# Kernel tuning notes

Measured on AMD Instinct MI355X. Metric: run time of the kernel, lower is better.

The kernel has to match this reference:

```python
import jax, jax.numpy as jnp
import numpy as np

B, L, HC, D = 4, 4096, 4, 1024
K, DIL = 4, 2
EPS = 1e-5
C = HC * D
PAD = (K - 1) * DIL


def setup_inputs() -> dict:
    key = jax.random.key(0)
    k1, k2, k3 = jax.random.split(key, 3)
    x = jax.random.normal(k1, (B, L, HC, D), dtype=jnp.float32)
    # RMSNorm affine weights, one per chunk (torch init: ones; randomize slightly for a
    # non-trivial baseline)
    norm_weight = 1.0 + 0.02 * jax.random.normal(k2, (HC, D), dtype=jnp.float32)
    # depthwise conv weight [C, 1, K] (torch init is zeros; use small random values so
    # the kernel-correctness baseline is non-degenerate)
    conv_weight = 0.1 * jax.random.normal(k3, (C, 1, K), dtype=jnp.float32)
    return {"x": x, "norm_weight": norm_weight, "conv_weight": conv_weight}


def reference(x, norm_weight, conv_weight):
    # per-chunk RMSNorm over last dim: [B, L, HC, D]
    ms = jnp.mean(jnp.square(x), axis=-1, keepdims=True)
    xn = x * jax.lax.rsqrt(ms + EPS) * norm_weight[None, None, :, :]
    # concat chunks along feature dim -> [B, L, C], then to [B, C, L]
    xc = xn.reshape(B, L, C).transpose(0, 2, 1)
    # depthwise dilated causal conv1d: left-pad (K-1)*DIL, output length L
    y = jax.lax.conv_general_dilated(
        xc, conv_weight,
        window_strides=(1,),
        padding=((PAD, 0),),
        rhs_dilation=(DIL,),
        feature_group_count=C,
        dimension_numbers=("NCH", "OIH", "NCH"),
    )
    y = jax.nn.silu(y)
    # back to [B, L, HC, D]
    return y.transpose(0, 2, 1).reshape(B, L, HC, D)
```

## Files before the change

### kernel.cpp

```cpp
#include <hip/hip_runtime.h>

namespace {

constexpr int B = 4, L = 4096, HC = 4, D = 1024, K = 4, DIL = 2;
constexpr int PAD = (K - 1) * DIL;
constexpr float EPS = 1e-5f;
constexpr int CL = 64;
constexpr int ST = 8;
constexpr int NSTEP = CL / ST;
constexpr int NT = L / CL;
constexpr int BDIM = 256;

__global__ __launch_bounds__(BDIM, 4) void engram_shortconv_stream(
    const float* __restrict__ x,
    const float* __restrict__ nw,
    const float* __restrict__ cw,
    float* __restrict__ out)
{
    __shared__ float s_part[ST][BDIM];
    __shared__ float s_inv[CL + PAD];

    const int blk = blockIdx.x;
    const int t   = blk % NT;
    const int hc  = (blk / NT) % HC;
    const int b   = blk / (NT * HC);
    const int l0  = t * CL;

    const int tid  = threadIdx.x;
    const int wave = tid >> 6;
    const int lane = tid & 63;

    const size_t rs = (size_t)HC * D;
    const float* xcol = x   + ((size_t)b * L * HC + (size_t)hc) * D + tid * 4;
    float*       ocol = out + ((size_t)b * L * HC + (size_t)hc) * D + tid * 4;

    const float4 nw4 = *(const float4*)(nw + (size_t)hc * D + tid * 4);
    const float nwv[4] = { nw4.x, nw4.y, nw4.z, nw4.w };
    float wk[4][4];
    #pragma unroll
    for (int j = 0; j < 4; ++j) {
        const float4 w = *(const float4*)(cw + ((size_t)hc * D + tid * 4 + j) * K);
        wk[j][0] = w.x * nwv[j]; wk[j][1] = w.y * nwv[j];
        wk[j][2] = w.z * nwv[j]; wk[j][3] = w.w * nwv[j];
    }

    float win[PAD][4];
    float pf[ST][4];

    #pragma unroll
    for (int r = 0; r < PAD; ++r) {
        const int l = l0 - PAD + r;
        float4 v = make_float4(0.f, 0.f, 0.f, 0.f);
        if (l >= 0) v = *(const float4*)(xcol + (size_t)l * rs);
        win[r][0] = v.x; win[r][1] = v.y; win[r][2] = v.z; win[r][3] = v.w;
    }
    #pragma unroll
    for (int r = 0; r < PAD; ++r)
        s_part[r][tid] = win[r][0]*win[r][0] + win[r][1]*win[r][1]
                       + win[r][2]*win[r][2] + win[r][3]*win[r][3];
    #pragma unroll
    for (int r = 0; r < ST; ++r) {
        const float4 v = *(const float4*)(xcol + (size_t)(l0 + r) * rs);
        pf[r][0] = v.x; pf[r][1] = v.y; pf[r][2] = v.z; pf[r][3] = v.w;
    }
    __syncthreads();
    for (int rr = wave; rr < PAD; rr += 4) {
        float s = s_part[rr][lane]       + s_part[rr][lane + 64]
                + s_part[rr][lane + 128] + s_part[rr][lane + 192];
        #pragma unroll
        for (int off = 32; off >= 1; off >>= 1) s += __shfl_xor(s, off);
        if (lane == 0) s_inv[rr] = rsqrtf(s * (1.0f / D) + EPS);
    }
    __syncthreads();
    #pragma unroll
    for (int r = 0; r < PAD; ++r) {
        const float iv = s_inv[r];
        win[r][0] *= iv; win[r][1] *= iv; win[r][2] *= iv; win[r][3] *= iv;
    }

    for (int s = 0; s < NSTEP; ++s) {
        const int base = l0 + s * ST;
        const int ib   = s * ST + PAD;

        #pragma unroll
        for (int r = 0; r < ST; ++r)
            s_part[r][tid] = pf[r][0]*pf[r][0] + pf[r][1]*pf[r][1]
                           + pf[r][2]*pf[r][2] + pf[r][3]*pf[r][3];
        __syncthreads();
        for (int rr = wave; rr < ST; rr += 4) {
            float sm = s_part[rr][lane]       + s_part[rr][lane + 64]
                     + s_part[rr][lane + 128] + s_part[rr][lane + 192];
            #pragma unroll
            for (int off = 32; off >= 1; off >>= 1) sm += __shfl_xor(sm, off);
            if (lane == 0) s_inv[ib + rr] = rsqrtf(sm * (1.0f / D) + EPS);
        }
        __syncthreads();

        #pragma unroll
        for (int r = 0; r < ST; ++r) {
            const float iv = s_inv[ib + r];
            pf[r][0] *= iv; pf[r][1] *= iv; pf[r][2] *= iv; pf[r][3] *= iv;
        }

        #pragma unroll
        for (int i = 0; i < ST; ++i) {
            float4 o; float* op = &o.x;
            #pragma unroll
            for (int j = 0; j < 4; ++j) {
                float a = 0.f;
                #pragma unroll
                for (int k = 0; k < 4; ++k) {
                    const int rel = i - 6 + 2 * k;
                    const float xv = (rel < 0) ? win[6 + rel][j] : pf[rel][j];
                    a = fmaf(wk[j][k], xv, a);
                }
                op[j] = a / (1.0f + __expf(-a));
            }
            *(float4*)(ocol + (size_t)(base + i) * rs) = o;
        }

        #pragma unroll
        for (int r = 0; r < PAD; ++r) {
            win[r][0] = pf[r + 2][0]; win[r][1] = pf[r + 2][1];
            win[r][2] = pf[r + 2][2]; win[r][3] = pf[r + 2][3];
        }

        if (s < NSTEP - 1) {
            #pragma unroll
            for (int r = 0; r < ST; ++r) {
                const float4 v = *(const float4*)(xcol + (size_t)(base + ST + r) * rs);
                pf[r][0] = v.x; pf[r][1] = v.y; pf[r][2] = v.z; pf[r][3] = v.w;
            }
        }
    }
}

}

extern "C" void kernel_launch(void* const* d_in, const int* in_sizes, int n_in,
                              void* d_out, int out_size, void* d_ws, size_t ws_size,
                              hipStream_t stream) {
    const float* x  = (const float*)d_in[0];
    const float* nw = (const float*)d_in[1];
    const float* cw = (const float*)d_in[2];
    float* out = (float*)d_out;

    const int nblocks = B * HC * NT;
    engram_shortconv_stream<<<dim3(nblocks), dim3(BDIM), 0, stream>>>(x, nw, cw, out);
}
```

Measured before the change: 111.3 us.

## Double-buffer register prefetch of input rows with lighter barriers and nontemporal stores

Loads are now prefetched two steps ahead into alternating register buffers (A/Bv), so global loads for step s+2 can be in flight while step s computes. __syncthreads is replaced by a custom barrier that waits only on LDS counters, so outstanding global loads no longer stall at barriers. Output is written with nontemporal stores, and the per-row inverse-RMS buffer is shrunk to a per-step array. The extra buffer roughly doubles live registers for prefetched data, which may reduce occupancy under the 4-blocks launch bound.

```diff
diff --git a/kernel.cpp b/kernel.cpp
--- a/kernel.cpp
+++ b/kernel.cpp
@@ -11,14 +11,22 @@
 constexpr int NT = L / CL;
 constexpr int BDIM = 256;
 
-__global__ __launch_bounds__(BDIM, 4) void engram_shortconv_stream(
+typedef float f32x4 __attribute__((ext_vector_type(4)));
+
+#define BLOCK_BARRIER() do {                                   \
+    asm volatile("s_waitcnt lgkmcnt(0)" ::: "memory");         \
+    __builtin_amdgcn_s_barrier();                              \
+    asm volatile("" ::: "memory");                             \
+} while (0)
+
+__global__ __launch_bounds__(BDIM, 4) void engram_shortconv_dbuf(
     const float* __restrict__ x,
     const float* __restrict__ nw,
     const float* __restrict__ cw,
     float* __restrict__ out)
 {
     __shared__ float s_part[ST][BDIM];
-    __shared__ float s_inv[CL + PAD];
+    __shared__ float s_invS[ST];
 
     const int blk = blockIdx.x;
     const int t   = blk % NT;
@@ -35,103 +43,143 @@
     float*       ocol = out + ((size_t)b * L * HC + (size_t)hc) * D + tid * 4;
 
     const float4 nw4 = *(const float4*)(nw + (size_t)hc * D + tid * 4);
-    const float nwv[4] = { nw4.x, nw4.y, nw4.z, nw4.w };
-    float wk[4][4];
+    float4 cwv[4];
     #pragma unroll
-    for (int j = 0; j < 4; ++j) {
-        const float4 w = *(const float4*)(cw + ((size_t)hc * D + tid * 4 + j) * K);
-        wk[j][0] = w.x * nwv[j]; wk[j][1] = w.y * nwv[j];
-        wk[j][2] = w.z * nwv[j]; wk[j][3] = w.w * nwv[j];
+    for (int j = 0; j < 4; ++j)
+        cwv[j] = *(const float4*)(cw + ((size_t)hc * D + tid * 4 + j) * K);
+
+    float win[PAD][4];
+    float A[ST][4], Bv[ST][4];
+    if (l0 >= PAD) {
+        #pragma unroll
+        for (int r = 0; r < PAD; ++r) {
+            const float4 v = *(const float4*)(xcol + (size_t)(l0 - PAD + r) * rs);
+            win[r][0] = v.x; win[r][1] = v.y; win[r][2] = v.z; win[r][3] = v.w;
+        }
+    } else {
+        #pragma unroll
+        for (int r = 0; r < PAD; ++r) {
+            const int l = l0 - PAD + r;
+            float4 v = make_float4(0.f, 0.f, 0.f, 0.f);
+            if (l >= 0) v = *(const float4*)(xcol + (size_t)l * rs);
+            win[r][0] = v.x; win[r][1] = v.y; win[r][2] = v.z; win[r][3] = v.w;
+        }
+    }
+    #pragma unroll
+    for (int r = 0; r < ST; ++r) {
+        const float4 v = *(const float4*)(xcol + (size_t)(l0 + r) * rs);
+        A[r][0] = v.x; A[r][1] = v.y; A[r][2] = v.z; A[r][3] = v.w;
+    }
+    #pragma unroll
+    for (int r = 0; r < ST; ++r) {
+        const float4 v = *(const float4*)(xcol + (size_t)(l0 + ST + r) * rs);
+        Bv[r][0] = v.x; Bv[r][1] = v.y; Bv[r][2] = v.z; Bv[r][3] = v.w;
     }
 
-    float win[PAD][4];
-    float pf[ST][4];
+    float wk[4][4];
+    {
+        const float gv[4] = { nw4.x, nw4.y, nw4.z, nw4.w };
+        #pragma unroll
+        for (int j = 0; j < 4; ++j) {
+            wk[j][0] = cwv[j].x * gv[j]; wk[j][1] = cwv[j].y * gv[j];
+            wk[j][2] = cwv[j].z * gv[j]; wk[j][3] = cwv[j].w * gv[j];
+        }
+    }
 
-    #pragma unroll
-    for (int r = 0; r < PAD; ++r) {
-        const int l = l0 - PAD + r;
-        float4 v = make_float4(0.f, 0.f, 0.f, 0.f);
-        if (l >= 0) v = *(const float4*)(xcol + (size_t)l * rs);
-        win[r][0] = v.x; win[r][1] = v.y; win[r][2] = v.z; win[r][3] = v.w;
-    }
     #pragma unroll
     for (int r = 0; r < PAD; ++r)
         s_part[r][tid] = win[r][0]*win[r][0] + win[r][1]*win[r][1]
                        + win[r][2]*win[r][2] + win[r][3]*win[r][3];
-    #pragma unroll
-    for (int r = 0; r < ST; ++r) {
-        const float4 v = *(const float4*)(xcol + (size_t)(l0 + r) * rs);
-        pf[r][0] = v.x; pf[r][1] = v.y; pf[r][2] = v.z; pf[r][3] = v.w;
-    }
-    __syncthreads();
-    for (int rr = wave; rr < PAD; rr += 4) {
+    BLOCK_BARRIER();
+    {
+        int rr = wave;
         float s = s_part[rr][lane]       + s_part[rr][lane + 64]
                 + s_part[rr][lane + 128] + s_part[rr][lane + 192];
         #pragma unroll
         for (int off = 32; off >= 1; off >>= 1) s += __shfl_xor(s, off);
-        if (lane == 0) s_inv[rr] = rsqrtf(s * (1.0f / D) + EPS);
+        if (lane == 0) s_invS[rr] = rsqrtf(s * (1.0f / D) + EPS);
+        rr = wave + 4;
+        if (rr < PAD) {
+            float s2 = s_part[rr][lane]       + s_part[rr][lane + 64]
+                     + s_part[rr][lane + 128] + s_part[rr][lane + 192];
+            #pragma unroll
+            for (int off = 32; off >= 1; off >>= 1) s2 += __shfl_xor(s2, off);
+            if (lane == 0) s_invS[rr] = rsqrtf(s2 * (1.0f / D) + EPS);
+        }
     }
-    __syncthreads();
+    BLOCK_BARRIER();
     #pragma unroll
     for (int r = 0; r < PAD; ++r) {
-        const float iv = s_inv[r];
+        const float iv = s_invS[r];
         win[r][0] *= iv; win[r][1] *= iv; win[r][2] *= iv; win[r][3] *= iv;
     }
+    BLOCK_BARRIER();
 
-    for (int s = 0; s < NSTEP; ++s) {
-        const int base = l0 + s * ST;
-        const int ib   = s * ST + PAD;
-
+    auto step = [&](float (&cur)[ST][4], int s) {
         #pragma unroll
         for (int r = 0; r < ST; ++r)
-            s_part[r][tid] = pf[r][0]*pf[r][0] + pf[r][1]*pf[r][1]
-                           + pf[r][2]*pf[r][2] + pf[r][3]*pf[r][3];
-        __syncthreads();
-        for (int rr = wave; rr < ST; rr += 4) {
-            float sm = s_part[rr][lane]       + s_part[rr][lane + 64]
+            s_part[r][tid] = cur[r][0]*cur[r][0] + cur[r][1]*cur[r][1]
+                           + cur[r][2]*cur[r][2] + cur[r][3]*cur[r][3];
+        BLOCK_BARRIER();
+        {
+            int rr = wave;
+            float s1 = s_part[rr][lane]       + s_part[rr][lane + 64]
                      + s_part[rr][lane + 128] + s_part[rr][lane + 192];
             #pragma unroll
-            for (int off = 32; off >= 1; off >>= 1) sm += __shfl_xor(sm, off);
-            if (lane == 0) s_inv[ib + rr] = rsqrtf(sm * (1.0f / D) + EPS);
+            for (int off = 32; off >= 1; off >>= 1) s1 += __shfl_xor(s1, off);
+            if (lane == 0) s_invS[rr] = rsqrtf(s1 * (1.0f / D) + EPS);
+            rr = wave + 4;
+            float s2 = s_part[rr][lane]       + s_part[rr][lane + 64]
+                     + s_part[rr][lane + 128] + s_part[rr][lane + 192];
+            #pragma unroll
+            for (int off = 32; off >= 1; off >>= 1) s2 += __shfl_xor(s2, off);
+            if (lane == 0) s_invS[rr] = rsqrtf(s2 * (1.0f / D) + EPS);
         }
-        __syncthreads();
+        BLOCK_BARRIER();
 
+        const int base = l0 + s * ST;
         #pragma unroll
         for (int r = 0; r < ST; ++r) {
-            const float iv = s_inv[ib + r];
-            pf[r][0] *= iv; pf[r][1] *= iv; pf[r][2] *= iv; pf[r][3] *= iv;
+            const float iv = s_invS[r];
+            cur[r][0] *= iv; cur[r][1] *= iv; cur[r][2] *= iv; cur[r][3] *= iv;
         }
 
         #pragma unroll
         for (int i = 0; i < ST; ++i) {
-            float4 o; float* op = &o.x;
+            float av[4];
             #pragma unroll
             for (int j = 0; j < 4; ++j) {
-                float a = 0.f;
+                float a = 0.0f;
                 #pragma unroll
                 for (int k = 0; k < 4; ++k) {
                     const int rel = i - 6 + 2 * k;
-                    const float xv = (rel < 0) ? win[6 + rel][j] : pf[rel][j];
+                    const float xv = (rel < 0) ? win[6 + rel][j] : cur[rel][j];
                     a = fmaf(wk[j][k], xv, a);
                 }
-                op[j] = a / (1.0f + __expf(-a));
+                av[j] = a / (1.0f + __expf(-a));
             }
-            *(float4*)(ocol + (size_t)(base + i) * rs) = o;
+            f32x4 o = { av[0], av[1], av[2], av[3] };
+            __builtin_nontemporal_store(o, (f32x4*)(ocol + (size_t)(base + i) * rs));
         }
 
         #pragma unroll
         for (int r = 0; r < PAD; ++r) {
-            win[r][0] = pf[r + 2][0]; win[r][1] = pf[r + 2][1];
-            win[r][2] = pf[r + 2][2]; win[r][3] = pf[r + 2][3];
+            win[r][0] = cur[r + 2][0]; win[r][1] = cur[r + 2][1];
+            win[r][2] = cur[r + 2][2]; win[r][3] = cur[r + 2][3];
         }
 
-        if (s < NSTEP - 1) {
+        if (s < NSTEP - 2) {
             #pragma unroll
             for (int r = 0; r < ST; ++r) {
-                const float4 v = *(const float4*)(xcol + (size_t)(base + ST + r) * rs);
-                pf[r][0] = v.x; pf[r][1] = v.y; pf[r][2] = v.z; pf[r][3] = v.w;
+                const float4 v = *(const float4*)(xcol + (size_t)(base + 2 * ST + r) * rs);
+                cur[r][0] = v.x; cur[r][1] = v.y; cur[r][2] = v.z; cur[r][3] = v.w;
             }
         }
+    };
+
+    for (int s2 = 0; s2 < NSTEP; s2 += 2) {
+        step(A, s2);
+        step(Bv, s2 + 1);
     }
 }
 
@@ -146,5 +194,5 @@
     float* out = (float*)d_out;
 
     const int nblocks = B * HC * NT;
-    engram_shortconv_stream<<<dim3(nblocks), dim3(BDIM), 0, stream>>>(x, nw, cw, out);
+    engram_shortconv_dbuf<<<dim3(nblocks), dim3(BDIM), 0, stream>>>(x, nw, cw, out);
 }
```

Result: slower. 135.3 us (+21.5%).
